# Kernel tuning notes

Measured on AMD Instinct MI355X. Metric: run time of the kernel, lower is better.

## Reference

```python
import jax, jax.numpy as jnp
import numpy as np
from jax import lax

KSIZE, SIGMA, ALPHA = 9, 7.0, 0.05
DN = ('NCHW', 'OIHW', 'NCHW')

def _sobel_weights():
    sx = np.array([[-1, 0, 1], [-2, 0, 2], [-1, 0, 1]], np.float32)
    sy = np.array([[-1, -2, -1], [0, 0, 0], [1, 2, 1]], np.float32)
    return jnp.asarray(np.stack([sx, sy])[:, None])  # (2,1,3,3)

def _gauss_weights():
    ax = np.arange(KSIZE, dtype=np.float32) - (KSIZE - 1) / 2.0
    g1 = np.exp(-(ax ** 2) / (2.0 * SIGMA ** 2))
    g2 = np.outer(g1, g1)
    g2 = g2 / g2.sum()
    return jnp.asarray(g2[None, None])  # (1,1,9,9)

def setup_inputs() -> dict:
    key = jax.random.key(0)
    x = jax.random.normal(key, (1, 1, 4096, 4096), dtype=jnp.float32)
    return {"x": x, "sobel_w": _sobel_weights(), "gauss_w": _gauss_weights()}

def reference(x, sobel_w, gauss_w):
    # Image gradients (Sobel, zero padding, cross-correlation like torch Conv2d)
    g = lax.conv_general_dilated(x, sobel_w, (1, 1), [(1, 1), (1, 1)], dimension_numbers=DN)  # (N,2,H,W)
    Ix, Iy = g[:, 0:1], g[:, 1:2]
    # Channel products Ixx, Iyy, Ixy
    prods = jnp.concatenate([Ix * Ix, Iy * Iy, Ix * Iy], axis=1)  # (N,3,H,W)
    # Second moment: same Gaussian applied per channel (depthwise)
    gk = jnp.tile(gauss_w, (3, 1, 1, 1))  # (3,1,9,9)
    pad = (KSIZE - 1) // 2
    S = lax.conv_general_dilated(prods, gk, (1, 1), [(pad, pad), (pad, pad)],
                                 feature_group_count=3, dimension_numbers=DN)
    Sxx, Syy, Sxy = S[:, 0:1], S[:, 1:2], S[:, 2:3]
    # Corner response R = det - alpha*trace^2
    tr = Sxx + Syy
    R = Sxx * Syy - Sxy * Sxy - ALPHA * tr * tr  # (N,1,H,W)
    # NMS: threshold below median (torch.median = lower middle element), 7x7 maxpool, keep maxima
    med = jnp.quantile(R, 0.5, method='lower')
    Rt = jnp.where(R > med, R, jnp.zeros_like(R))
    pooled = lax.reduce_window(Rt, -jnp.inf, lax.max, (1, 1, 7, 7), (1, 1, 1, 1),
                               [(0, 0), (0, 0), (3, 3), (3, 3)])
    mask = jnp.where(Rt == pooled, jnp.ones_like(Rt), jnp.zeros_like(Rt))
    return mask * Rt
```

## Files before the change

kernel.cpp:

```cpp
#include <hip/hip_runtime.h>
#include <math.h>

#define HW 4096
#define NPIX (HW * HW)
#define N4 (NPIX / 4)
#define TS 32
#define MED_RANK 8388607u
#define NOBIN 0xFFFFFFFFu
#define H1_COPIES 16
#define H23_COPIES 4

typedef unsigned int u32;
typedef unsigned long long u64;

__device__ __forceinline__ u32 f2key(float f) {
  u32 u = __float_as_uint(f);
  return (u & 0x80000000u) ? ~u : (u | 0x80000000u);
}

__device__ __forceinline__ void wave_hist_add(u32* lh, u32 bin) {
  int lane = threadIdx.x & 63;
  u32 prev = __shfl_up(bin, 1);
  bool head = (lane == 0) || (prev != bin);
  u64 hb = __ballot(head);
  u64 after = (lane < 63) ? (hb >> (lane + 1)) : 0ull;
  int run = after ? __ffsll((long long)after) : (64 - lane);
  if (head && bin != NOBIN) atomicAdd(&lh[bin], (u32)run);
}

template <int RT, bool POOL>
__global__ __launch_bounds__(256, 4) void harris_main(
    const float* __restrict__ x, const float* __restrict__ gw,
    const u32* __restrict__ sel, float* __restrict__ Rout,
    u32* __restrict__ h1) {
  constexpr int PR = RT + 8;
  constexpr int XR = RT + 10;
  constexpr int CGR = (RT + 3) / 4;
  constexpr int VP = ((((CGR - 1) * 4 + 12) + 3) / 4) * 4 + 4;
  constexpr int RTD = POOL ? RT : 1;
  constexpr int NH = POOL ? 1 : 1024;
  constexpr int XIN_F = XR * (XR + 2);
  constexpr int V_F = 3 * RT * VP;
  constexpr int UNI_F = (XIN_F > V_F) ? XIN_F : V_F;

  __shared__ __align__(16) float uni[UNI_F];
  __shared__ float p0[PR][PR], p1[PR][PR], p2[PR][PR];
  __shared__ float g1s[12];
  __shared__ float rt[RTD][RTD + 2];
  __shared__ float hm[RTD][TS];
  __shared__ u32 lh[NH];

  float(*xin)[XR + 2] = (float(*)[XR + 2])uni;
  float(*v)[VP] = (float(*)[VP])uni;

  const int tid = threadIdx.x;
  const int or0 = blockIdx.y * TS - (POOL ? 3 : 0);
  const int oc0 = blockIdx.x * TS - (POOL ? 3 : 0);
  const int xr0 = or0 - 5, xc0 = oc0 - 5;

  if constexpr (!POOL)
    for (int i = tid; i < NH; i += 256) lh[i] = 0u;

  if (tid < 9) {
    float s = 0.f;
#pragma unroll
    for (int j = 0; j < 9; ++j) s += gw[tid * 9 + j];
    g1s[tid] = s;
  }

  for (int idx = tid; idx < XR * XR; idx += 256) {
    int r = idx / XR, c = idx % XR;
    int gr = xr0 + r, gc = xc0 + c;
    float val = 0.f;
    if ((u32)gr < (u32)HW && (u32)gc < (u32)HW) val = x[(size_t)gr * HW + gc];
    xin[r][c] = val;
  }
  __syncthreads();

  if constexpr (!POOL) {
    for (int task = tid; task < PR * (PR / 4); task += 256) {
      int r = task / (PR / 4);
      int c4 = (task % (PR / 4)) * 4;
      int gr = or0 - 4 + r;
      int gc0 = oc0 - 4 + c4;
      __align__(16) float a[3][8];
#pragma unroll
      for (int rr = 0; rr < 3; ++rr) {
        *(float4*)&a[rr][0] = *(const float4*)&xin[r + rr][c4];
        *(float4*)&a[rr][4] = *(const float4*)&xin[r + rr][c4 + 4];
      }
      float4 P0, P1, P2;
      float* p0v = (float*)&P0;
      float* p1v = (float*)&P1;
      float* p2v = (float*)&P2;
#pragma unroll
      for (int o = 0; o < 4; ++o) {
        float Ix = (a[0][o + 2] - a[0][o]) + 2.f * (a[1][o + 2] - a[1][o]) +
                   (a[2][o + 2] - a[2][o]);
        float Iy = (a[2][o] - a[0][o]) + 2.f * (a[2][o + 1] - a[0][o + 1]) +
                   (a[2][o + 2] - a[0][o + 2]);
        bool in = ((u32)gr < (u32)HW) && ((u32)(gc0 + o) < (u32)HW);
        p0v[o] = in ? Ix * Ix : 0.f;
        p1v[o] = in ? Iy * Iy : 0.f;
        p2v[o] = in ? Ix * Iy : 0.f;
      }
      *(float4*)&p0[r][c4] = P0;
      *(float4*)&p1[r][c4] = P1;
      *(float4*)&p2[r][c4] = P2;
    }
  } else {
    for (int idx = tid; idx < PR * PR; idx += 256) {
      int r = idx / PR, c = idx % PR;
      int gr = or0 - 4 + r, gc = oc0 - 4 + c;
      float P0 = 0.f, P1 = 0.f, P2 = 0.f;
      if ((u32)gr < (u32)HW && (u32)gc < (u32)HW) {
        float a00 = xin[r][c], a01 = xin[r][c + 1], a02 = xin[r][c + 2];
        float a10 = xin[r + 1][c], a12 = xin[r + 1][c + 2];
        float a20 = xin[r + 2][c], a21 = xin[r + 2][c + 1],
              a22 = xin[r + 2][c + 2];
        float Ix = (a02 - a00) + 2.f * (a12 - a10) + (a22 - a20);
        float Iy = (a20 - a00) + 2.f * (a21 - a01) + (a22 - a02);
        P0 = Ix * Ix;
        P1 = Iy * Iy;
        P2 = Ix * Iy;
      }
      p0[r][c] = P0;
      p1[r][c] = P1;
      p2[r][c] = P2;
    }
  }
  __syncthreads();

  float g[9];
#pragma unroll
  for (int k = 0; k < 9; ++k) g[k] = g1s[k];

  if constexpr (!POOL) {
    for (int task = tid; task < 3 * (RT / 8) * PR; task += 256) {
      int ch = task / ((RT / 8) * PR);
      int rem = task % ((RT / 8) * PR);
      int rg = (rem / PR) * 8;
      int c = rem % PR;
      const float(*pp)[PR] = (ch == 0) ? p0 : (ch == 1) ? p1 : p2;
      float col[16];
#pragma unroll
      for (int k = 0; k < 16; ++k) col[k] = pp[rg + k][c];
#pragma unroll
      for (int o = 0; o < 8; ++o) {
        float s = 0.f;
#pragma unroll
        for (int k = 0; k < 9; ++k) s = fmaf(g[k], col[o + k], s);
        v[ch * RT + rg + o][c] = s;
      }
    }
  } else {
    for (int task = tid; task < 3 * CGR * PR; task += 256) {
      int ch = task / (CGR * PR);
      int rem = task % (CGR * PR);
      int rg = (rem / PR) * 4;
      int c = rem % PR;
      const float(*pp)[PR] = (ch == 0) ? p0 : (ch == 1) ? p1 : p2;
      float col[12];
#pragma unroll
      for (int k = 0; k < 12; ++k) col[k] = (rg + k < PR) ? pp[rg + k][c] : 0.f;
#pragma unroll
      for (int o = 0; o < 4; ++o) {
        int rv = rg + o;
        if (rv < RT) {
          float s = 0.f;
#pragma unroll
          for (int k = 0; k < 9; ++k) s = fmaf(g[k], col[o + k], s);
          v[ch * RT + rv][c] = s;
        }
      }
    }
  }
  __syncthreads();

  float med = 0.f;
  if (POOL) med = __uint_as_float(sel[2]);

  for (int task = tid; task < RT * CGR; task += 256) {
    int r = task / CGR;
    int c0i = (task % CGR) * 4;
    float s3[3][4];
#pragma unroll
    for (int ch = 0; ch < 3; ++ch) {
      const float4* vp = (const float4*)&v[ch * RT + r][c0i];
      float4 w0 = vp[0], w1 = vp[1], w2 = vp[2];
      float row[12] = {w0.x, w0.y, w0.z, w0.w, w1.x, w1.y,
                       w1.z, w1.w, w2.x, w2.y, w2.z, w2.w};
#pragma unroll
      for (int o = 0; o < 4; ++o) {
        float s = 0.f;
#pragma unroll
        for (int k = 0; k < 9; ++k) s = fmaf(g[k], row[o + k], s);
        s3[ch][o] = s;
      }
    }
    if constexpr (!POOL) {
      float4 rv4;
      float* rp = (float*)&rv4;
#pragma unroll
      for (int o = 0; o < 4; ++o) {
        float Sxx = s3[0][o], Syy = s3[1][o], Sxy = s3[2][o];
        float tr = Sxx + Syy;
        rp[o] = Sxx * Syy - Sxy * Sxy - 0.05f * tr * tr;
      }
      *(float4*)&Rout[(size_t)(or0 + r) * HW + (oc0 + c0i)] = rv4;
#pragma unroll
      for (int o = 0; o < 4; ++o) wave_hist_add(lh, f2key(rp[o]) >> 22);
    } else {
#pragma unroll
      for (int o = 0; o < 4; ++o) {
        int c = c0i + o;
        if (c < RT) {
          float Sxx = s3[0][o], Syy = s3[1][o], Sxy = s3[2][o];
          float tr = Sxx + Syy;
          float Rv = Sxx * Syy - Sxy * Sxy - 0.05f * tr * tr;
          int gr = or0 + r, gc = oc0 + c;
          float val = -INFINITY;
          if ((u32)gr < (u32)HW && (u32)gc < (u32)HW)
            val = (Rv > med) ? Rv : 0.f;
          rt[r][c] = val;
        }
      }
    }
  }

  if constexpr (!POOL) {
    __syncthreads();
    const u32 cp = (u32)(blockIdx.y * gridDim.x + blockIdx.x) & (H1_COPIES - 1);
    u32* dst = h1 + cp * NH;
    for (int i = tid; i < NH; i += 256) {
      u32 c = lh[i];
      if (c) atomicAdd(&dst[i], c);
    }
  }

  if constexpr (POOL) {
    __syncthreads();
    for (int idx = tid; idx < RT * TS; idx += 256) {
      int r = idx / TS, c = idx % TS;
      float m = rt[r][c];
#pragma unroll
      for (int k = 1; k < 7; ++k) m = fmaxf(m, rt[r][c + k]);
      hm[r][c] = m;
    }
    __syncthreads();
    for (int idx = tid; idx < TS * TS; idx += 256) {
      int r = idx / TS, c = idx % TS;
      float pooled = hm[r][c];
#pragma unroll
      for (int k = 1; k < 7; ++k) pooled = fmaxf(pooled, hm[r + k][c]);
      float rc = rt[r + 3][c + 3];
      Rout[(size_t)(or0 + 3 + r) * HW + (oc0 + 3 + c)] =
          (rc == pooled) ? rc : 0.f;
    }
  }
}

__global__ __launch_bounds__(256) void hist_pass2(
    const float4* __restrict__ R4, const u32* __restrict__ sel,
    u32* __restrict__ hist) {
  __shared__ u32 lh[4096];
  for (int i = threadIdx.x; i < 4096; i += 256) lh[i] = 0u;
  const u32 p10 = sel[1] >> 22;
  __syncthreads();
  const u32 stride = gridDim.x * 256;
  for (u32 i = blockIdx.x * 256 + threadIdx.x; i < N4; i += stride) {
    float4 f = R4[i];
    const float* fp = (const float*)&f;
#pragma unroll
    for (int j = 0; j < 4; ++j) {
      u32 k = f2key(fp[j]);
      wave_hist_add(lh, ((k >> 22) == p10) ? ((k >> 10) & 0xFFFu) : NOBIN);
    }
  }
  __syncthreads();
  u32* dst = hist + (blockIdx.x & (H23_COPIES - 1)) * 4096;
  for (int i = threadIdx.x; i < 4096; i += 256) {
    u32 c = lh[i];
    if (c) atomicAdd(&dst[i], c);
  }
}

__global__ __launch_bounds__(256) void hist_pass3(
    const float4* __restrict__ R4, const u32* __restrict__ sel,
    u32* __restrict__ hist) {
  __shared__ u32 lh[1024];
  for (int i = threadIdx.x; i < 1024; i += 256) lh[i] = 0u;
  const u32 p22 = sel[1] >> 10;
  __syncthreads();
  const u32 stride = gridDim.x * 256;
  for (u32 i = blockIdx.x * 256 + threadIdx.x; i < N4; i += stride) {
    float4 f = R4[i];
    const float* fp = (const float*)&f;
#pragma unroll
    for (int j = 0; j < 4; ++j) {
      u32 k = f2key(fp[j]);
      if ((k >> 10) == p22) atomicAdd(&lh[k & 0x3FFu], 1u);
    }
  }
  __syncthreads();
  u32* dst = hist + (blockIdx.x & (H23_COPIES - 1)) * 1024;
  for (int i = threadIdx.x; i < 1024; i += 256) {
    u32 c = lh[i];
    if (c) atomicAdd(&dst[i], c);
  }
}

template <int NBINS, int NCOPY, int SHIFT, bool FIRST, bool LAST>
__global__ __launch_bounds__(256) void scan_select(const u32* __restrict__ hist,
                                                   u32* __restrict__ sel) {
  __shared__ u32 part[256];
  constexpr int C = NBINS / 256;
  int tid = threadIdx.x;
  u32 s = 0;
  for (int i = 0; i < C; ++i) {
    u32 b = 0;
#pragma unroll
    for (int cp = 0; cp < NCOPY; ++cp) b += hist[cp * NBINS + tid * C + i];
    s += b;
  }
  part[tid] = s;
  __syncthreads();
  if (tid == 0) {
    u32 r = FIRST ? MED_RANK : sel[0];
    u32 cum = 0;
    int seg = 0;
    for (; seg < 255; ++seg) {
      u32 ps = part[seg];
      if (cum + ps > r) break;
      cum += ps;
    }
    int b = seg * C;
    for (int i = 0; i < C; ++i) {
      u32 h = 0;
#pragma unroll
      for (int cp = 0; cp < NCOPY; ++cp) h += hist[cp * NBINS + b];
      if (cum + h > r) break;
      cum += h;
      ++b;
    }
    sel[0] = r - cum;
    u32 pfx = (FIRST ? 0u : sel[1]) | ((u32)b << SHIFT);
    sel[1] = pfx;
    if (LAST)
      sel[2] = (pfx & 0x80000000u) ? (pfx ^ 0x80000000u) : ~pfx;
  }
}

__global__ __launch_bounds__(256) void final_pool(const float* __restrict__ R,
                                                  const u32* __restrict__ sel,
                                                  float* __restrict__ out) {
  __shared__ __align__(16) float rt[38][44];
  __shared__ float hm[38][32];
  const float med = __uint_as_float(sel[2]);
  const int r0 = blockIdx.y * TS - 3;
  const int c0 = blockIdx.x * TS;
  const int c0m4 = c0 - 4;
  for (int idx = threadIdx.x; idx < 38 * 10; idx += 256) {
    int r = idx / 10, j = idx % 10;
    int gr = r0 + r, gc = c0m4 + 4 * j;
    float4 v4;
    float* vp = (float*)&v4;
    if ((u32)gr < (u32)HW && gc >= 0 && gc + 3 < HW) {
      float4 Rv = *(const float4*)&R[(size_t)gr * HW + gc];
      v4.x = (Rv.x > med) ? Rv.x : 0.f;
      v4.y = (Rv.y > med) ? Rv.y : 0.f;
      v4.z = (Rv.z > med) ? Rv.z : 0.f;
      v4.w = (Rv.w > med) ? Rv.w : 0.f;
    } else {
#pragma unroll
      for (int t = 0; t < 4; ++t) {
        int g2 = gc + t;
        float val = -INFINITY;
        if ((u32)gr < (u32)HW && (u32)g2 < (u32)HW) {
          float Rv = R[(size_t)gr * HW + g2];
          val = (Rv > med) ? Rv : 0.f;
        }
        vp[t] = val;
      }
    }
    *(float4*)&rt[r][4 * j] = v4;
  }
  __syncthreads();
  for (int idx = threadIdx.x; idx < 38 * TS; idx += 256) {
    int r = idx / TS, c = idx % TS;
    float m = rt[r][c + 1];
#pragma unroll
    for (int k = 2; k < 8; ++k) m = fmaxf(m, rt[r][c + k]);
    hm[r][c] = m;
  }
  __syncthreads();
  for (int idx = threadIdx.x; idx < TS * TS; idx += 256) {
    int r = idx / TS, c = idx % TS;
    float pooled = hm[r][c];
#pragma unroll
    for (int k = 1; k < 7; ++k) pooled = fmaxf(pooled, hm[r + k][c]);
    float rc = rt[r + 3][c + 4];
    out[(size_t)(r0 + 3 + r) * HW + (c0 + c)] = (rc == pooled) ? rc : 0.f;
  }
}

extern "C" void kernel_launch(void* const* d_in, const int* in_sizes, int n_in,
                              void* d_out, int out_size, void* d_ws,
                              size_t ws_size, hipStream_t stream) {
  (void)in_sizes;
  (void)n_in;
  (void)out_size;
  const float* x = (const float*)d_in[0];
  const float* gw = (const float*)d_in[2];
  float* out = (float*)d_out;

  const size_t RB = (size_t)NPIX * sizeof(float);
  const size_t HN = H1_COPIES * 1024 + H23_COPIES * 4096 + H23_COPIES * 1024 + 8;
  const size_t HB = HN * sizeof(u32);
  const bool planA = ws_size >= RB + HB;

  float* Rbuf;
  u32* hb;
  if (planA) {
    Rbuf = (float*)d_ws;
    hb = (u32*)((char*)d_ws + RB);
  } else {
    Rbuf = out;
    hb = (u32*)d_ws;
  }
  u32* h1 = hb;
  u32* h2 = h1 + H1_COPIES * 1024;
  u32* h3 = h2 + H23_COPIES * 4096;
  u32* sel = h3 + H23_COPIES * 1024;

  dim3 grid(HW / TS, HW / TS);
  hipMemsetAsync(hb, 0, HB, stream);
  harris_main<32, false><<<grid, 256, 0, stream>>>(x, gw, nullptr, Rbuf, h1);
  scan_select<1024, H1_COPIES, 22, true, false><<<1, 256, 0, stream>>>(h1, sel);
  hist_pass2<<<1024, 256, 0, stream>>>((const float4*)Rbuf, sel, h2);
  scan_select<4096, H23_COPIES, 10, false, false><<<1, 256, 0, stream>>>(h2, sel);
  hist_pass3<<<1024, 256, 0, stream>>>((const float4*)Rbuf, sel, h3);
  scan_select<1024, H23_COPIES, 0, false, true><<<1, 256, 0, stream>>>(h3, sel);
  if (planA) {
    final_pool<<<grid, 256, 0, stream>>>(Rbuf, sel, out);
  } else {
    harris_main<38, true><<<grid, 256, 0, stream>>>(x, gw, sel, out, nullptr);
  }
}
```

Before: 308.0 us.

## Compact median-candidate keys in pass 2 and specialize interior tiles

During the second histogram pass, keys whose top 10 bits match the selected bucket are also written into per-stripe compaction buffers in spare workspace. The third pass then histograms only those compacted keys instead of rereading the whole 64 MB R buffer, and falls back to the full scan if any stripe overflowed. The main kernel also takes a bounds-check-free path for interior tiles and reworks the vertical Gaussian pass to process float4 column groups per thread. The cost is extra atomics and scattered global writes in pass 2, plus a dependence on how much workspace is available.

```diff
diff --git a/kernel.cpp b/kernel.cpp
--- a/kernel.cpp
+++ b/kernel.cpp
@@ -9,6 +9,7 @@
 #define NOBIN 0xFFFFFFFFu
 #define H1_COPIES 16
 #define H23_COPIES 4
+#define NSTRIPE 64
 
 typedef unsigned int u32;
 typedef unsigned long long u64;
@@ -57,6 +58,8 @@
   const int or0 = blockIdx.y * TS - (POOL ? 3 : 0);
   const int oc0 = blockIdx.x * TS - (POOL ? 3 : 0);
   const int xr0 = or0 - 5, xc0 = oc0 - 5;
+  const bool inter =
+      (xr0 >= 0) && (xc0 >= 0) && (xr0 + XR <= HW) && (xc0 + XR <= HW);
 
   if constexpr (!POOL)
     for (int i = tid; i < NH; i += 256) lh[i] = 0u;
@@ -68,12 +71,19 @@
     g1s[tid] = s;
   }
 
-  for (int idx = tid; idx < XR * XR; idx += 256) {
-    int r = idx / XR, c = idx % XR;
-    int gr = xr0 + r, gc = xc0 + c;
-    float val = 0.f;
-    if ((u32)gr < (u32)HW && (u32)gc < (u32)HW) val = x[(size_t)gr * HW + gc];
-    xin[r][c] = val;
+  if (inter) {
+    for (int idx = tid; idx < XR * XR; idx += 256) {
+      int r = idx / XR, c = idx % XR;
+      xin[r][c] = x[(size_t)(xr0 + r) * HW + (xc0 + c)];
+    }
+  } else {
+    for (int idx = tid; idx < XR * XR; idx += 256) {
+      int r = idx / XR, c = idx % XR;
+      int gr = xr0 + r, gc = xc0 + c;
+      float val = 0.f;
+      if ((u32)gr < (u32)HW && (u32)gc < (u32)HW) val = x[(size_t)gr * HW + gc];
+      xin[r][c] = val;
+    }
   }
   __syncthreads();
 
@@ -81,8 +91,6 @@
     for (int task = tid; task < PR * (PR / 4); task += 256) {
       int r = task / (PR / 4);
       int c4 = (task % (PR / 4)) * 4;
-      int gr = or0 - 4 + r;
-      int gc0 = oc0 - 4 + c4;
       __align__(16) float a[3][8];
 #pragma unroll
       for (int rr = 0; rr < 3; ++rr) {
@@ -93,16 +101,31 @@
       float* p0v = (float*)&P0;
       float* p1v = (float*)&P1;
       float* p2v = (float*)&P2;
-#pragma unroll
-      for (int o = 0; o < 4; ++o) {
-        float Ix = (a[0][o + 2] - a[0][o]) + 2.f * (a[1][o + 2] - a[1][o]) +
-                   (a[2][o + 2] - a[2][o]);
-        float Iy = (a[2][o] - a[0][o]) + 2.f * (a[2][o + 1] - a[0][o + 1]) +
-                   (a[2][o + 2] - a[0][o + 2]);
-        bool in = ((u32)gr < (u32)HW) && ((u32)(gc0 + o) < (u32)HW);
-        p0v[o] = in ? Ix * Ix : 0.f;
-        p1v[o] = in ? Iy * Iy : 0.f;
-        p2v[o] = in ? Ix * Iy : 0.f;
+      if (inter) {
+#pragma unroll
+        for (int o = 0; o < 4; ++o) {
+          float Ix = (a[0][o + 2] - a[0][o]) + 2.f * (a[1][o + 2] - a[1][o]) +
+                     (a[2][o + 2] - a[2][o]);
+          float Iy = (a[2][o] - a[0][o]) + 2.f * (a[2][o + 1] - a[0][o + 1]) +
+                     (a[2][o + 2] - a[0][o + 2]);
+          p0v[o] = Ix * Ix;
+          p1v[o] = Iy * Iy;
+          p2v[o] = Ix * Iy;
+        }
+      } else {
+        int gr = or0 - 4 + r;
+        int gc0 = oc0 - 4 + c4;
+#pragma unroll
+        for (int o = 0; o < 4; ++o) {
+          float Ix = (a[0][o + 2] - a[0][o]) + 2.f * (a[1][o + 2] - a[1][o]) +
+                     (a[2][o + 2] - a[2][o]);
+          float Iy = (a[2][o] - a[0][o]) + 2.f * (a[2][o + 1] - a[0][o + 1]) +
+                     (a[2][o + 2] - a[0][o + 2]);
+          bool in = ((u32)gr < (u32)HW) && ((u32)(gc0 + o) < (u32)HW);
+          p0v[o] = in ? Ix * Ix : 0.f;
+          p1v[o] = in ? Iy * Iy : 0.f;
+          p2v[o] = in ? Ix * Iy : 0.f;
+        }
       }
       *(float4*)&p0[r][c4] = P0;
       *(float4*)&p1[r][c4] = P1;
@@ -136,21 +159,27 @@
   for (int k = 0; k < 9; ++k) g[k] = g1s[k];
 
   if constexpr (!POOL) {
-    for (int task = tid; task < 3 * (RT / 8) * PR; task += 256) {
-      int ch = task / ((RT / 8) * PR);
-      int rem = task % ((RT / 8) * PR);
-      int rg = (rem / PR) * 8;
-      int c = rem % PR;
+    if (tid < 240) {
+      int ch = tid / 80;
+      int rem = tid - ch * 80;
+      int rg = (rem / 10) * 4;
+      int c4 = (rem % 10) * 4;
       const float(*pp)[PR] = (ch == 0) ? p0 : (ch == 1) ? p1 : p2;
-      float col[16];
-#pragma unroll
-      for (int k = 0; k < 16; ++k) col[k] = pp[rg + k][c];
-#pragma unroll
-      for (int o = 0; o < 8; ++o) {
-        float s = 0.f;
-#pragma unroll
-        for (int k = 0; k < 9; ++k) s = fmaf(g[k], col[o + k], s);
-        v[ch * RT + rg + o][c] = s;
+      float4 col[12];
+#pragma unroll
+      for (int k = 0; k < 12; ++k) col[k] = *(const float4*)&pp[rg + k][c4];
+#pragma unroll
+      for (int o = 0; o < 4; ++o) {
+        float4 s = {0.f, 0.f, 0.f, 0.f};
+#pragma unroll
+        for (int k = 0; k < 9; ++k) {
+          float4 cv = col[o + k];
+          s.x = fmaf(g[k], cv.x, s.x);
+          s.y = fmaf(g[k], cv.y, s.y);
+          s.z = fmaf(g[k], cv.z, s.z);
+          s.w = fmaf(g[k], cv.w, s.w);
+        }
+        *(float4*)&v[ch * RT + rg + o][c4] = s;
       }
     }
   } else {
@@ -262,19 +291,49 @@
 
 __global__ __launch_bounds__(256) void hist_pass2(
     const float4* __restrict__ R4, const u32* __restrict__ sel,
-    u32* __restrict__ hist) {
+    u32* __restrict__ hist, u32* __restrict__ wcnt, u32* __restrict__ cbuf,
+    u32 segcap) {
   __shared__ u32 lh[4096];
   for (int i = threadIdx.x; i < 4096; i += 256) lh[i] = 0u;
   const u32 p10 = sel[1] >> 22;
   __syncthreads();
+  const int lane = threadIdx.x & 63;
+  const u32 stripe = ((blockIdx.x << 2) + (threadIdx.x >> 6)) & (NSTRIPE - 1);
+  u32* seg = cbuf + (size_t)stripe * segcap;
   const u32 stride = gridDim.x * 256;
   for (u32 i = blockIdx.x * 256 + threadIdx.x; i < N4; i += stride) {
     float4 f = R4[i];
     const float* fp = (const float*)&f;
+    u32 k[4];
+    bool mt[4];
 #pragma unroll
     for (int j = 0; j < 4; ++j) {
-      u32 k = f2key(fp[j]);
-      wave_hist_add(lh, ((k >> 22) == p10) ? ((k >> 10) & 0xFFFu) : NOBIN);
+      k[j] = f2key(fp[j]);
+      mt[j] = (k[j] >> 22) == p10;
+    }
+#pragma unroll
+    for (int j = 0; j < 4; ++j)
+      wave_hist_add(lh, mt[j] ? ((k[j] >> 10) & 0xFFFu) : NOBIN);
+    if (segcap) {
+      u32 m = (u32)mt[0] + (u32)mt[1] + (u32)mt[2] + (u32)mt[3];
+      u32 scan = m;
+#pragma unroll
+      for (int d = 1; d < 64; d <<= 1) {
+        u32 t = __shfl_up(scan, d);
+        if (lane >= d) scan += t;
+      }
+      u32 tot = __shfl(scan, 63);
+      if (tot) {
+        u32 base = 0;
+        if (lane == 0) base = atomicAdd(&wcnt[stripe], tot);
+        base = __shfl(base, 0);
+        u32 pos = base + scan - m;
+        u32 o1 = (u32)mt[0], o2 = o1 + (u32)mt[1], o3 = o2 + (u32)mt[2];
+        if (mt[0] && pos < segcap) seg[pos] = k[0];
+        if (mt[1] && pos + o1 < segcap) seg[pos + o1] = k[1];
+        if (mt[2] && pos + o2 < segcap) seg[pos + o2] = k[2];
+        if (mt[3] && pos + o3 < segcap) seg[pos + o3] = k[3];
+      }
     }
   }
   __syncthreads();
@@ -287,19 +346,47 @@
 
 __global__ __launch_bounds__(256) void hist_pass3(
     const float4* __restrict__ R4, const u32* __restrict__ sel,
+    const u32* __restrict__ wcnt, const u32* __restrict__ cbuf, u32 segcap,
     u32* __restrict__ hist) {
   __shared__ u32 lh[1024];
   for (int i = threadIdx.x; i < 1024; i += 256) lh[i] = 0u;
   const u32 p22 = sel[1] >> 10;
-  __syncthreads();
-  const u32 stride = gridDim.x * 256;
-  for (u32 i = blockIdx.x * 256 + threadIdx.x; i < N4; i += stride) {
-    float4 f = R4[i];
-    const float* fp = (const float*)&f;
-#pragma unroll
-    for (int j = 0; j < 4; ++j) {
-      u32 k = f2key(fp[j]);
-      if ((k >> 10) == p22) atomicAdd(&lh[k & 0x3FFu], 1u);
+  bool useC = (segcap > 0);
+#pragma unroll 8
+  for (int s = 0; s < NSTRIPE; ++s)
+    if (wcnt[s] > segcap) useC = false;
+  __syncthreads();
+  if (useC) {
+    const u32 s = blockIdx.x & (NSTRIPE - 1);
+    const u32 chunk = blockIdx.x >> 6;
+    const u32 n = wcnt[s];
+    const u32 clen = (n + 15) >> 4;
+    const u32 start = chunk * clen;
+    const u32 end = (start + clen < n) ? (start + clen) : n;
+    const u32* seg = cbuf + (size_t)s * segcap;
+    if (start < end) {
+      u32 span = end - start;
+      u32 nit = (span + 255) >> 8;
+      for (u32 it = 0; it < nit; ++it) {
+        u32 i = start + it * 256 + threadIdx.x;
+        u32 bin = NOBIN;
+        if (i < end) {
+          u32 k = seg[i];
+          bin = ((k >> 10) == p22) ? (k & 0x3FFu) : NOBIN;
+        }
+        wave_hist_add(lh, bin);
+      }
+    }
+  } else {
+    const u32 stride = gridDim.x * 256;
+    for (u32 i = blockIdx.x * 256 + threadIdx.x; i < N4; i += stride) {
+      float4 f = R4[i];
+      const float* fp = (const float*)&f;
+#pragma unroll
+      for (int j = 0; j < 4; ++j) {
+        u32 k = f2key(fp[j]);
+        if ((k >> 10) == p22) atomicAdd(&lh[k & 0x3FFu], 1u);
+      }
     }
   }
   __syncthreads();
@@ -415,7 +502,8 @@
   float* out = (float*)d_out;
 
   const size_t RB = (size_t)NPIX * sizeof(float);
-  const size_t HN = H1_COPIES * 1024 + H23_COPIES * 4096 + H23_COPIES * 1024 + 8;
+  const size_t HN =
+      H1_COPIES * 1024 + H23_COPIES * 4096 + H23_COPIES * 1024 + 8 + NSTRIPE;
   const size_t HB = HN * sizeof(u32);
   const bool planA = ws_size >= RB + HB;
 
@@ -432,14 +520,29 @@
   u32* h2 = h1 + H1_COPIES * 1024;
   u32* h3 = h2 + H23_COPIES * 4096;
   u32* sel = h3 + H23_COPIES * 1024;
+  u32* wcnt = sel + 8;
+
+  u32 segcap = 0;
+  u32* cbuf = nullptr;
+  const size_t used = (planA ? RB : 0) + HB;
+  if (planA && ws_size > used + 4096) {
+    size_t spare = (ws_size - used) / sizeof(u32);
+    size_t sc = spare / NSTRIPE;
+    if (sc > (size_t)(NPIX / NSTRIPE)) sc = NPIX / NSTRIPE;
+    segcap = (u32)sc;
+    cbuf = (u32*)((char*)d_ws + used);
+  }
 
   dim3 grid(HW / TS, HW / TS);
   hipMemsetAsync(hb, 0, HB, stream);
   harris_main<32, false><<<grid, 256, 0, stream>>>(x, gw, nullptr, Rbuf, h1);
   scan_select<1024, H1_COPIES, 22, true, false><<<1, 256, 0, stream>>>(h1, sel);
-  hist_pass2<<<1024, 256, 0, stream>>>((const float4*)Rbuf, sel, h2);
-  scan_select<4096, H23_COPIES, 10, false, false><<<1, 256, 0, stream>>>(h2, sel);
-  hist_pass3<<<1024, 256, 0, stream>>>((const float4*)Rbuf, sel, h3);
+  hist_pass2<<<1024, 256, 0, stream>>>((const float4*)Rbuf, sel, h2, wcnt, cbuf,
+                                       segcap);
+  scan_select<4096, H23_COPIES, 10, false, false><<<1, 256, 0, stream>>>(h2,
+                                                                         sel);
+  hist_pass3<<<1024, 256, 0, stream>>>((const float4*)Rbuf, sel, wcnt, cbuf,
+                                       segcap, h3);
   scan_select<1024, H23_COPIES, 0, false, true><<<1, 256, 0, stream>>>(h3, sel);
   if (planA) {
     final_pool<<<grid, 256, 0, stream>>>(Rbuf, sel, out);
```

Measured after the change: 577.8 us. +87.6%, slower.
